# Performance work log

Measured on AMD Instinct MI355X. Metric: run time of the kernel, lower is better.

Reference implementation:

```python
import jax, jax.numpy as jnp
import numpy as np

B, T, I, H, C = 4096, 512, 3, 32, 3  # batch, seq_len, input, hidden, classes


def setup_inputs() -> dict:
    key = jax.random.key(0)
    ks = jax.random.split(key, 7)
    s = 1.0 / np.sqrt(H)  # PyTorch LSTM init scale
    return {
        "x": jax.random.normal(ks[0], (B, T, I), dtype=jnp.float32),
        "W_ih": jax.random.normal(ks[1], (4 * H, I), dtype=jnp.float32) * s,
        "W_hh": jax.random.normal(ks[2], (4 * H, H), dtype=jnp.float32) * s,
        "b_ih": jax.random.normal(ks[3], (4 * H,), dtype=jnp.float32) * s,
        "b_hh": jax.random.normal(ks[4], (4 * H,), dtype=jnp.float32) * s,
        "W_fc": jax.random.normal(ks[5], (C, H), dtype=jnp.float32) * s,
        "b_fc": jax.random.normal(ks[6], (C,), dtype=jnp.float32) * s,
    }


def reference(x, W_ih, W_hh, b_ih, b_hh, W_fc, b_fc):
    # Precompute input contribution to all gates for every timestep: (B,T,4H)
    xg = jnp.einsum("bti,gi->btg", x, W_ih) + b_ih + b_hh
    h0 = jnp.zeros((x.shape[0], H), dtype=x.dtype)
    c0 = jnp.zeros_like(h0)

    def step(carry, xt):
        h, c = carry
        g = xt + h @ W_hh.T  # (B,4H)
        i_g, f_g, g_g, o_g = jnp.split(g, 4, axis=-1)  # PyTorch gate order i,f,g,o
        i_g = jax.nn.sigmoid(i_g)
        f_g = jax.nn.sigmoid(f_g)
        g_g = jnp.tanh(g_g)
        o_g = jax.nn.sigmoid(o_g)
        c = f_g * c + i_g * g_g
        h = o_g * jnp.tanh(c)
        return (h, c), None

    (h_last, _), _ = jax.lax.scan(step, (h0, c0), jnp.swapaxes(xg, 0, 1))
    return h_last @ W_fc.T + b_fc  # (B, num_classes)
```

## Files before the change

### kernel.cpp

```cpp
#include <hip/hip_runtime.h>
#include <cstdint>

#define B_TOT 4096
#define T_LEN 512
#define CHUNK 256
#define LOG2E 1.44269504088896340736f
#define HSTR  40

typedef _Float16 f16x8 __attribute__((ext_vector_type(8)));
typedef _Float16 f16x4 __attribute__((ext_vector_type(4)));
typedef float    f32x4 __attribute__((ext_vector_type(4)));

__device__ __forceinline__ float ex2(float v)  { return __builtin_amdgcn_exp2f(v); }
__device__ __forceinline__ float rcp_(float v) { return __builtin_amdgcn_rcpf(v); }

__global__ __launch_bounds__(256, 2)
void lstm_pr(const float* __restrict__ x,
             const float* __restrict__ W_ih,
             const float* __restrict__ W_hh,
             const float* __restrict__ b_ih,
             const float* __restrict__ b_hh,
             const float* __restrict__ W_fc,
             const float* __restrict__ b_fc,
             float* __restrict__ out)
{
    __shared__ __align__(16) _Float16 hbuf[2][8][HSTR];
    __shared__ __align__(16) _Float16 xbuf[CHUNK / 2][8][8];

    const int tid  = threadIdx.x;
    const int wave = tid >> 6;
    const int lane = tid & 63;
    const int n    = lane & 15;
    const int kq   = lane >> 4;
    const int nb   = n & 7;
    const int tb   = blockIdx.x * 8;

    const int   gate_m = n & 3;
    const int   hl_m   = n >> 2;
    const int   R1     = gate_m * 32 + 8 * wave + hl_m;
    const int   R2     = R1 + 4;
    const float sm     = (gate_m == 2) ? (-2.0f * LOG2E) : (-LOG2E);

    f16x8 aW1, aW2;
#pragma unroll
    for (int j = 0; j < 8; ++j) {
        aW1[j] = (_Float16)(sm * W_hh[R1 * 32 + 8 * kq + j]);
        aW2[j] = (_Float16)(sm * W_hh[R2 * 32 + 8 * kq + j]);
    }
    f16x8 a21 = {}, a22 = {};
    if (kq == 0) {
        a21[0] = (_Float16)(sm * W_ih[R1 * 3 + 0]);
        a21[1] = (_Float16)(sm * W_ih[R1 * 3 + 1]);
        a21[2] = (_Float16)(sm * W_ih[R1 * 3 + 2]);
        a21[3] = (_Float16)(sm * (b_ih[R1] + b_hh[R1]));
        a22[0] = (_Float16)(sm * W_ih[R2 * 3 + 0]);
        a22[1] = (_Float16)(sm * W_ih[R2 * 3 + 1]);
        a22[2] = (_Float16)(sm * W_ih[R2 * 3 + 2]);
        a22[3] = (_Float16)(sm * (b_ih[R2] + b_hh[R2]));
    }

    const int hid_s = 8 * wave + kq + ((n >> 3) ? 4 : 0);

    if (tid < 160) ((int*)&hbuf[0][0][0])[tid] = 0;

    const float K2 = -2.0f * LOG2E;
    float c = 0.0f;
    const f32x4 z = {0.f, 0.f, 0.f, 0.f};
    f32x4 accx1, accx2;

    const bool hi = (n >> 3) != 0;

    for (int tc = 0; tc < T_LEN; tc += CHUNK) {
#pragma unroll
        for (int s = 0; s < 8; ++s) {
            const int idx = tid + s * 256;
            const int tl = idx >> 3, m = idx & 7;
            const float* xp = x + ((size_t)(tb + m) * T_LEN + (tc + tl)) * 3;
            f16x4 v;
            v[0] = (_Float16)xp[0]; v[1] = (_Float16)xp[1];
            v[2] = (_Float16)xp[2]; v[3] = (_Float16)1.0f;
            *(f16x4*)&xbuf[tl >> 1][m][4 * (tl & 1)] = v;
        }
        __syncthreads();

        f16x8 xp = *(const f16x8*)&xbuf[0][nb][0];
        {
            const f16x8 b2 = __builtin_shufflevector(xp, xp, 0, 1, 2, 3, 0, 1, 2, 3);
            accx1 = __builtin_amdgcn_mfma_f32_16x16x32_f16(a21, b2, z, 0, 0, 0);
            accx2 = __builtin_amdgcn_mfma_f32_16x16x32_f16(a22, b2, z, 0, 0, 0);
        }

        for (int t2 = 0; t2 < CHUNK / 2; ++t2) {
            {
                const f16x8 bh = *(const f16x8*)&hbuf[0][nb][8 * kq];
                const f32x4 ac1 = __builtin_amdgcn_mfma_f32_16x16x32_f16(aW1, bh, accx1, 0, 0, 0);
                const f32x4 ac2 = __builtin_amdgcn_mfma_f32_16x16x32_f16(aW2, bh, accx2, 0, 0, 0);

                const float a0 = hi ? ac2[0] : ac1[0];
                const float a1 = hi ? ac2[1] : ac1[1];
                const float a2 = hi ? ac2[2] : ac1[2];
                const float a3 = hi ? ac2[3] : ac1[3];

                const float ei = ex2(a0), ef = ex2(a1), eg = ex2(a2), eo = ex2(a3);
                const float pi = 1.0f + ei, pf = 1.0f + ef, pg = 1.0f + eg;
                const float mg = 1.0f - eg;
                const float pp = pi * pg, qn = mg * pf;
                c = fmaf(c, pp, qn) * rcp_(pf * pp);
                const float ec = ex2(c * K2);
                const float po = 1.0f + eo, pc = 1.0f + ec, mc = 1.0f - ec;
                const float h = mc * rcp_(po * pc);
                hbuf[1][nb][hid_s] = (_Float16)h;

                const f16x8 b2 = __builtin_shufflevector(xp, xp, 4, 5, 6, 7, 4, 5, 6, 7);
                accx1 = __builtin_amdgcn_mfma_f32_16x16x32_f16(a21, b2, z, 0, 0, 0);
                accx2 = __builtin_amdgcn_mfma_f32_16x16x32_f16(a22, b2, z, 0, 0, 0);
            }
            __syncthreads();

            {
                const f16x8 bh = *(const f16x8*)&hbuf[1][nb][8 * kq];
                const int t2n = (t2 + 1) & (CHUNK / 2 - 1);
                const f16x8 xpN = *(const f16x8*)&xbuf[t2n][nb][0];

                const f32x4 ac1 = __builtin_amdgcn_mfma_f32_16x16x32_f16(aW1, bh, accx1, 0, 0, 0);
                const f32x4 ac2 = __builtin_amdgcn_mfma_f32_16x16x32_f16(aW2, bh, accx2, 0, 0, 0);

                const float a0 = hi ? ac2[0] : ac1[0];
                const float a1 = hi ? ac2[1] : ac1[1];
                const float a2 = hi ? ac2[2] : ac1[2];
                const float a3 = hi ? ac2[3] : ac1[3];

                const float ei = ex2(a0), ef = ex2(a1), eg = ex2(a2), eo = ex2(a3);
                const float pi = 1.0f + ei, pf = 1.0f + ef, pg = 1.0f + eg;
                const float mg = 1.0f - eg;
                const float pp = pi * pg, qn = mg * pf;
                c = fmaf(c, pp, qn) * rcp_(pf * pp);
                const float ec = ex2(c * K2);
                const float po = 1.0f + eo, pc = 1.0f + ec, mc = 1.0f - ec;
                const float h = mc * rcp_(po * pc);
                hbuf[0][nb][hid_s] = (_Float16)h;

                const f16x8 b2 = __builtin_shufflevector(xpN, xpN, 0, 1, 2, 3, 0, 1, 2, 3);
                accx1 = __builtin_amdgcn_mfma_f32_16x16x32_f16(a21, b2, z, 0, 0, 0);
                accx2 = __builtin_amdgcn_mfma_f32_16x16x32_f16(a22, b2, z, 0, 0, 0);
                xp = xpN;
            }
            __syncthreads();
        }
    }

    if (tid < 24) {
        const int m = tid / 3, cc = tid % 3;
        float acc = b_fc[cc];
#pragma unroll
        for (int k = 0; k < 32; ++k)
            acc = fmaf(W_fc[cc * 32 + k], (float)hbuf[0][m][k], acc);
        out[(tb + m) * 3 + cc] = acc;
    }
}

extern "C" void kernel_launch(void* const* d_in, const int* in_sizes, int n_in,
                              void* d_out, int out_size, void* d_ws, size_t ws_size,
                              hipStream_t stream) {
    const float* x    = (const float*)d_in[0];
    const float* W_ih = (const float*)d_in[1];
    const float* W_hh = (const float*)d_in[2];
    const float* b_ih = (const float*)d_in[3];
    const float* b_hh = (const float*)d_in[4];
    const float* W_fc = (const float*)d_in[5];
    const float* b_fc = (const float*)d_in[6];
    float* out = (float*)d_out;

    dim3 grid(B_TOT / 8);
    dim3 block(256);
    lstm_pr<<<grid, block, 0, stream>>>(x, W_ih, W_hh, b_ih, b_hh, W_fc, b_fc, out);
}
```

Before: 184.6 us.

## Unroll LSTM loop by four, drop x shuffles, add setprio and stagger blocks

The recurrence loop is unrolled to four timesteps per iteration. The per-step shufflevector of the x operand is replaced by separate even/odd input-weight A fragments (a1e/a1o), so the packed x vector feeds the MFMA directly. Each step's MFMA-plus-activation critical section is wrapped in s_setprio(1)/s_setprio(0) to favour the recurrent chain when waves compete. A short dummy rcp delay on blocks with blockIdx bit 8 set staggers co-resident blocks so their phases interleave; this adds a little dead work and more code size in exchange.

```diff
diff --git a/kernel.cpp b/kernel.cpp
--- a/kernel.cpp
+++ b/kernel.cpp
@@ -15,14 +15,14 @@
 __device__ __forceinline__ float rcp_(float v) { return __builtin_amdgcn_rcpf(v); }
 
 __global__ __launch_bounds__(256, 2)
-void lstm_pr(const float* __restrict__ x,
-             const float* __restrict__ W_ih,
-             const float* __restrict__ W_hh,
-             const float* __restrict__ b_ih,
-             const float* __restrict__ b_hh,
-             const float* __restrict__ W_fc,
-             const float* __restrict__ b_fc,
-             float* __restrict__ out)
+void lstm_pr2(const float* __restrict__ x,
+              const float* __restrict__ W_ih,
+              const float* __restrict__ W_hh,
+              const float* __restrict__ b_ih,
+              const float* __restrict__ b_hh,
+              const float* __restrict__ W_fc,
+              const float* __restrict__ b_fc,
+              float* __restrict__ out)
 {
     __shared__ __align__(16) _Float16 hbuf[2][8][HSTR];
     __shared__ __align__(16) _Float16 xbuf[CHUNK / 2][8][8];
@@ -47,107 +47,105 @@
         aW1[j] = (_Float16)(sm * W_hh[R1 * 32 + 8 * kq + j]);
         aW2[j] = (_Float16)(sm * W_hh[R2 * 32 + 8 * kq + j]);
     }
-    f16x8 a21 = {}, a22 = {};
+    f16x8 a1e = {}, a2e = {}, a1o = {}, a2o = {};
     if (kq == 0) {
-        a21[0] = (_Float16)(sm * W_ih[R1 * 3 + 0]);
-        a21[1] = (_Float16)(sm * W_ih[R1 * 3 + 1]);
-        a21[2] = (_Float16)(sm * W_ih[R1 * 3 + 2]);
-        a21[3] = (_Float16)(sm * (b_ih[R1] + b_hh[R1]));
-        a22[0] = (_Float16)(sm * W_ih[R2 * 3 + 0]);
-        a22[1] = (_Float16)(sm * W_ih[R2 * 3 + 1]);
-        a22[2] = (_Float16)(sm * W_ih[R2 * 3 + 2]);
-        a22[3] = (_Float16)(sm * (b_ih[R2] + b_hh[R2]));
+        const _Float16 w10 = (_Float16)(sm * W_ih[R1 * 3 + 0]);
+        const _Float16 w11 = (_Float16)(sm * W_ih[R1 * 3 + 1]);
+        const _Float16 w12 = (_Float16)(sm * W_ih[R1 * 3 + 2]);
+        const _Float16 w1b = (_Float16)(sm * (b_ih[R1] + b_hh[R1]));
+        const _Float16 w20 = (_Float16)(sm * W_ih[R2 * 3 + 0]);
+        const _Float16 w21 = (_Float16)(sm * W_ih[R2 * 3 + 1]);
+        const _Float16 w22 = (_Float16)(sm * W_ih[R2 * 3 + 2]);
+        const _Float16 w2b = (_Float16)(sm * (b_ih[R2] + b_hh[R2]));
+        a1e[0] = w10; a1e[1] = w11; a1e[2] = w12; a1e[3] = w1b;
+        a2e[0] = w20; a2e[1] = w21; a2e[2] = w22; a2e[3] = w2b;
+        a1o[4] = w10; a1o[5] = w11; a1o[6] = w12; a1o[7] = w1b;
+        a2o[4] = w20; a2o[5] = w21; a2o[6] = w22; a2o[7] = w2b;
     }
 
     const int hid_s = 8 * wave + kq + ((n >> 3) ? 4 : 0);
+    const bool hi   = (n >> 3) != 0;
 
     if (tid < 160) ((int*)&hbuf[0][0][0])[tid] = 0;
+
+    if (blockIdx.x & 256) {
+        float dly = (float)(lane + 1);
+#pragma unroll
+        for (int i = 0; i < 12; ++i) dly = rcp_(dly) + 1.0f;
+        asm volatile("" :: "v"(dly));
+    }
 
     const float K2 = -2.0f * LOG2E;
     float c = 0.0f;
     const f32x4 z = {0.f, 0.f, 0.f, 0.f};
     f32x4 accx1, accx2;
 
-    const bool hi = (n >> 3) != 0;
+#define LSTM_STEP(RP, WP)                                                      \
+    {                                                                          \
+        __builtin_amdgcn_s_setprio(1);                                         \
+        const f16x8 bh = *(const f16x8*)&hbuf[RP][nb][8 * kq];                 \
+        const f32x4 ac1 = __builtin_amdgcn_mfma_f32_16x16x32_f16(aW1, bh, accx1, 0, 0, 0); \
+        const f32x4 ac2 = __builtin_amdgcn_mfma_f32_16x16x32_f16(aW2, bh, accx2, 0, 0, 0); \
+        const float a0 = hi ? ac2[0] : ac1[0];                                 \
+        const float a1 = hi ? ac2[1] : ac1[1];                                 \
+        const float a2 = hi ? ac2[2] : ac1[2];                                 \
+        const float a3 = hi ? ac2[3] : ac1[3];                                 \
+        const float ei = ex2(a0), ef = ex2(a1), eg = ex2(a2), eo = ex2(a3);    \
+        const float pi = 1.0f + ei, pf = 1.0f + ef, pg = 1.0f + eg;            \
+        const float mg = 1.0f - eg;                                            \
+        const float pp = pi * pg, qn = mg * pf;                                \
+        c = fmaf(c, pp, qn) * rcp_(pf * pp);                                   \
+        const float ec = ex2(c * K2);                                          \
+        const float po = 1.0f + eo, pc = 1.0f + ec, mc = 1.0f - ec;            \
+        hbuf[WP][nb][hid_s] = (_Float16)(mc * rcp_(po * pc));                  \
+        __builtin_amdgcn_s_setprio(0);                                         \
+    }
 
     for (int tc = 0; tc < T_LEN; tc += CHUNK) {
 #pragma unroll
         for (int s = 0; s < 8; ++s) {
             const int idx = tid + s * 256;
             const int tl = idx >> 3, m = idx & 7;
-            const float* xp = x + ((size_t)(tb + m) * T_LEN + (tc + tl)) * 3;
+            const float* xp_ = x + ((size_t)(tb + m) * T_LEN + (tc + tl)) * 3;
             f16x4 v;
-            v[0] = (_Float16)xp[0]; v[1] = (_Float16)xp[1];
-            v[2] = (_Float16)xp[2]; v[3] = (_Float16)1.0f;
+            v[0] = (_Float16)xp_[0]; v[1] = (_Float16)xp_[1];
+            v[2] = (_Float16)xp_[2]; v[3] = (_Float16)1.0f;
             *(f16x4*)&xbuf[tl >> 1][m][4 * (tl & 1)] = v;
         }
         __syncthreads();
 
-        f16x8 xp = *(const f16x8*)&xbuf[0][nb][0];
-        {
-            const f16x8 b2 = __builtin_shufflevector(xp, xp, 0, 1, 2, 3, 0, 1, 2, 3);
-            accx1 = __builtin_amdgcn_mfma_f32_16x16x32_f16(a21, b2, z, 0, 0, 0);
-            accx2 = __builtin_amdgcn_mfma_f32_16x16x32_f16(a22, b2, z, 0, 0, 0);
-        }
+        f16x8 xpA = *(const f16x8*)&xbuf[0][nb][0];
+        accx1 = __builtin_amdgcn_mfma_f32_16x16x32_f16(a1e, xpA, z, 0, 0, 0);
+        accx2 = __builtin_amdgcn_mfma_f32_16x16x32_f16(a2e, xpA, z, 0, 0, 0);
 
-        for (int t2 = 0; t2 < CHUNK / 2; ++t2) {
-            {
-                const f16x8 bh = *(const f16x8*)&hbuf[0][nb][8 * kq];
-                const f32x4 ac1 = __builtin_amdgcn_mfma_f32_16x16x32_f16(aW1, bh, accx1, 0, 0, 0);
-                const f32x4 ac2 = __builtin_amdgcn_mfma_f32_16x16x32_f16(aW2, bh, accx2, 0, 0, 0);
+        for (int t4 = 0; t4 < CHUNK / 4; ++t4) {
+            const int base = 2 * t4;
+            const f16x8 xpB = *(const f16x8*)&xbuf[base + 1][nb][0];
 
-                const float a0 = hi ? ac2[0] : ac1[0];
-                const float a1 = hi ? ac2[1] : ac1[1];
-                const float a2 = hi ? ac2[2] : ac1[2];
-                const float a3 = hi ? ac2[3] : ac1[3];
-
-                const float ei = ex2(a0), ef = ex2(a1), eg = ex2(a2), eo = ex2(a3);
-                const float pi = 1.0f + ei, pf = 1.0f + ef, pg = 1.0f + eg;
-                const float mg = 1.0f - eg;
-                const float pp = pi * pg, qn = mg * pf;
-                c = fmaf(c, pp, qn) * rcp_(pf * pp);
-                const float ec = ex2(c * K2);
-                const float po = 1.0f + eo, pc = 1.0f + ec, mc = 1.0f - ec;
-                const float h = mc * rcp_(po * pc);
-                hbuf[1][nb][hid_s] = (_Float16)h;
-
-                const f16x8 b2 = __builtin_shufflevector(xp, xp, 4, 5, 6, 7, 4, 5, 6, 7);
-                accx1 = __builtin_amdgcn_mfma_f32_16x16x32_f16(a21, b2, z, 0, 0, 0);
-                accx2 = __builtin_amdgcn_mfma_f32_16x16x32_f16(a22, b2, z, 0, 0, 0);
-            }
+            LSTM_STEP(0, 1);
+            accx1 = __builtin_amdgcn_mfma_f32_16x16x32_f16(a1o, xpA, z, 0, 0, 0);
+            accx2 = __builtin_amdgcn_mfma_f32_16x16x32_f16(a2o, xpA, z, 0, 0, 0);
             __syncthreads();
 
-            {
-                const f16x8 bh = *(const f16x8*)&hbuf[1][nb][8 * kq];
-                const int t2n = (t2 + 1) & (CHUNK / 2 - 1);
-                const f16x8 xpN = *(const f16x8*)&xbuf[t2n][nb][0];
+            LSTM_STEP(1, 0);
+            accx1 = __builtin_amdgcn_mfma_f32_16x16x32_f16(a1e, xpB, z, 0, 0, 0);
+            accx2 = __builtin_amdgcn_mfma_f32_16x16x32_f16(a2e, xpB, z, 0, 0, 0);
+            __syncthreads();
 
-                const f32x4 ac1 = __builtin_amdgcn_mfma_f32_16x16x32_f16(aW1, bh, accx1, 0, 0, 0);
-                const f32x4 ac2 = __builtin_amdgcn_mfma_f32_16x16x32_f16(aW2, bh, accx2, 0, 0, 0);
+            const f16x8 xpAn = *(const f16x8*)&xbuf[(base + 2) & (CHUNK / 2 - 1)][nb][0];
+            LSTM_STEP(0, 1);
+            accx1 = __builtin_amdgcn_mfma_f32_16x16x32_f16(a1o, xpB, z, 0, 0, 0);
+            accx2 = __builtin_amdgcn_mfma_f32_16x16x32_f16(a2o, xpB, z, 0, 0, 0);
+            __syncthreads();
 
-                const float a0 = hi ? ac2[0] : ac1[0];
-                const float a1 = hi ? ac2[1] : ac1[1];
-                const float a2 = hi ? ac2[2] : ac1[2];
-                const float a3 = hi ? ac2[3] : ac1[3];
-
-                const float ei = ex2(a0), ef = ex2(a1), eg = ex2(a2), eo = ex2(a3);
-                const float pi = 1.0f + ei, pf = 1.0f + ef, pg = 1.0f + eg;
-                const float mg = 1.0f - eg;
-                const float pp = pi * pg, qn = mg * pf;
-                c = fmaf(c, pp, qn) * rcp_(pf * pp);
-                const float ec = ex2(c * K2);
-                const float po = 1.0f + eo, pc = 1.0f + ec, mc = 1.0f - ec;
-                const float h = mc * rcp_(po * pc);
-                hbuf[0][nb][hid_s] = (_Float16)h;
-
-                const f16x8 b2 = __builtin_shufflevector(xpN, xpN, 0, 1, 2, 3, 0, 1, 2, 3);
-                accx1 = __builtin_amdgcn_mfma_f32_16x16x32_f16(a21, b2, z, 0, 0, 0);
-                accx2 = __builtin_amdgcn_mfma_f32_16x16x32_f16(a22, b2, z, 0, 0, 0);
-                xp = xpN;
-            }
+            LSTM_STEP(1, 0);
+            accx1 = __builtin_amdgcn_mfma_f32_16x16x32_f16(a1e, xpAn, z, 0, 0, 0);
+            accx2 = __builtin_amdgcn_mfma_f32_16x16x32_f16(a2e, xpAn, z, 0, 0, 0);
+            xpA = xpAn;
             __syncthreads();
         }
     }
+#undef LSTM_STEP
 
     if (tid < 24) {
         const int m = tid / 3, cc = tid % 3;
@@ -173,5 +171,5 @@
 
     dim3 grid(B_TOT / 8);
     dim3 block(256);
-    lstm_pr<<<grid, block, 0, stream>>>(x, W_ih, W_hh, b_ih, b_hh, W_fc, b_fc, out);
+    lstm_pr2<<<grid, block, 0, stream>>>(x, W_ih, W_hh, b_ih, b_hh, W_fc, b_fc, out);
 }
```

Measured after the change: 168.2 us. -8.9%, faster.
